# Kernel tuning notes

Hardware: AMD Instinct MI355X
Metric: run time of the kernel (lower is better)

Reference implementation:

```python
import jax, jax.numpy as jnp
import numpy as np

EPS = 1e-12

def _l2norm(x):
    # normalize rows so dot product == cosine similarity
    return x / jnp.maximum(jnp.linalg.norm(x, axis=-1, keepdims=True), EPS)

def setup_inputs() -> dict:
    key = jax.random.key(0)
    k1, k2 = jax.random.split(key)
    source_feats = jax.random.normal(k1, (4096, 1024), dtype=jnp.float32)
    target_feats = jax.random.normal(k2, (65536, 1024), dtype=jnp.float32)
    return {"source_feats": source_feats, "target_feats": target_feats, "k": 4}

def reference(source_feats, target_feats, k):
    # cosine kNN matching: for each source frame, find k nearest target frames
    # by cosine distance, then average the (raw) target features.
    sn = _l2norm(source_feats)           # [N, d]
    tn = _l2norm(target_feats)           # [M, d]
    sim = sn @ tn.T                      # [N, M] cosine similarity (dist = 1 - sim)
    _, idx = jax.lax.top_k(sim, k)       # [N, k] highest similarity == smallest cosine distance
    neighbors = target_feats[idx]        # [N, k, d] gather
    out = neighbors.mean(axis=1)         # [N, d]
    return out
```

## Files before the change

kernel.cpp:

```cpp
#include <hip/hip_runtime.h>
#include <math.h>
#include <stdint.h>

#define M     4096
#define NTGT  65536
#define KD    1024

#define NS    32
#define SLICE (NTGT / NS)
#define BT    256
#define BS    256
#define NTILE (SLICE / BT)
#define TSTEP 16
#define TOTST (NTILE * TSTEP)
#define NCAND 256
#define RESC  32
#define BUFSZ 32768

typedef __attribute__((ext_vector_type(4)))  int i32x4;
typedef __attribute__((ext_vector_type(16))) int i32x16;

__device__ __forceinline__ char f2i8(float x) {
    int t = __float2int_rn(x);
    t = t > 127 ? 127 : (t < -127 ? -127 : t);
    return (char)t;
}

template <int NK>
__device__ __forceinline__ void insert_desc_u(uint32_t (&arr)[NK], uint32_t pk) {
    uint32_t cur = pk;
#pragma unroll
    for (int s = 0; s < NK; ++s) {
        uint32_t old = arr[s];
        bool g = cur > old;
        arr[s] = g ? cur : old;
        cur    = g ? old : cur;
    }
}

__device__ __forceinline__ void gload16(const void* g, void* l) {
    __builtin_amdgcn_global_load_lds(
        (const __attribute__((address_space(1))) unsigned int*)g,
        (__attribute__((address_space(3))) unsigned int*)l, 16, 0, 0);
}

__global__ void prep_targets(const float* __restrict__ T, float* __restrict__ tinv,
                             char* __restrict__ Tq) {
    const int wave = threadIdx.x >> 6;
    const int lane = threadIdx.x & 63;
    const int row  = blockIdx.x * 4 + wave;
    const float* p = T + (size_t)row * KD;
    float4 v[4];
    float s = 0.f;
#pragma unroll
    for (int j = 0; j < 4; ++j) {
        v[j] = *reinterpret_cast<const float4*>(p + lane * 4 + j * 256);
        s += v[j].x * v[j].x + v[j].y * v[j].y + v[j].z * v[j].z + v[j].w * v[j].w;
    }
#pragma unroll
    for (int off = 32; off; off >>= 1) s += __shfl_xor(s, off);
    const float rinv = 1.0f / sqrtf(fmaxf(s, 1e-24f));
    if (lane == 0) tinv[row] = rinv;
    const float sc = rinv * 1024.0f;
#pragma unroll
    for (int j = 0; j < 4; ++j) {
        char4 o;
        o.x = f2i8(v[j].x * sc); o.y = f2i8(v[j].y * sc);
        o.z = f2i8(v[j].z * sc); o.w = f2i8(v[j].w * sc);
        *reinterpret_cast<char4*>(Tq + (size_t)row * KD + lane * 4 + j * 256) = o;
    }
}

__global__ void prep_source(const float* __restrict__ S, char* __restrict__ Sq) {
    const int wave = threadIdx.x >> 6;
    const int lane = threadIdx.x & 63;
    const int row  = blockIdx.x * 4 + wave;
    const float* p = S + (size_t)row * KD;
#pragma unroll
    for (int j = 0; j < 4; ++j) {
        float4 v = *reinterpret_cast<const float4*>(p + lane * 4 + j * 256);
        char4 o;
        o.x = f2i8(v.x * 32.0f); o.y = f2i8(v.y * 32.0f);
        o.z = f2i8(v.z * 32.0f); o.w = f2i8(v.w * 32.0f);
        *reinterpret_cast<char4*>(Sq + (size_t)row * KD + lane * 4 + j * 256) = o;
    }
}

__global__ __launch_bounds__(512, 2)
void screen_kernel(const char* __restrict__ Sq, const char* __restrict__ Tq,
                   uint32_t* __restrict__ cand_out) {
    __shared__ __align__(16) unsigned char lds[2 * BUFSZ];

    const int tid  = threadIdx.x;
    const int lane = tid & 63, wid = tid >> 6;
    const int wr = wid >> 2, wc = wid & 3;
    const int l31 = lane & 31, l5 = lane >> 5;
    const int bx = blockIdx.x;
    const int by = blockIdx.y;
    const int sb   = bx * BS;
    const int tgt0 = by * SLICE;

    const int srow = tid >> 2;
    const int scol = ((tid & 3) ^ ((tid >> 3) & 3)) * 16;
    const char* aStage = Tq + (size_t)(tgt0 + srow) * KD + scol;
    const char* bStage = Sq + (size_t)(sb   + srow) * KD + scol;

    const int s3 = (l31 >> 1) & 3;
    int aOff0[4], aOff1[4], bOff0[2], bOff1[2];
#pragma unroll
    for (int m = 0; m < 4; ++m) {
        const int base = (wr * 128 + m * 32 + l31) * 64;
        aOff0[m] = base + ((l5    ) ^ s3) * 16;
        aOff1[m] = base + ((2 + l5) ^ s3) * 16;
    }
#pragma unroll
    for (int nt = 0; nt < 2; ++nt) {
        const int base = 16384 + (wc * 64 + nt * 32 + l31) * 64;
        bOff0[nt] = base + ((l5    ) ^ s3) * 16;
        bOff1[nt] = base + ((2 + l5) ^ s3) * 16;
    }

#define BARX()  __builtin_amdgcn_s_barrier()
#define FENCE() asm volatile("" ::: "memory")
#define VM4()   asm volatile("s_waitcnt vmcnt(4)" ::: "memory")
#define VM0()   asm volatile("s_waitcnt vmcnt(0)" ::: "memory")

#define STAGE(s_) do {                                                         \
        const int tt_ = (s_) >> 4, ks_ = (s_) & 15;                            \
        unsigned char* d_ = lds + (((s_) & 1) ? BUFSZ : 0) + tid * 16;         \
        const char* a_ = aStage + (size_t)(tt_ * BT) * KD + ks_ * 64;          \
        const char* b_ = bStage + ks_ * 64;                                    \
        gload16(a_,            d_);                                            \
        gload16(a_ + 128 * KD, d_ + 8192);                                     \
        gload16(b_,            d_ + 16384);                                    \
        gload16(b_ + 128 * KD, d_ + 16384 + 8192);                             \
    } while (0)

    uint32_t cand[2][8];
#pragma unroll
    for (int nt = 0; nt < 2; ++nt)
#pragma unroll
        for (int j = 0; j < 8; ++j) cand[nt][j] = 0u;

    STAGE(0);

#pragma unroll 1
    for (int tt = 0; tt < NTILE; ++tt) {
        i32x16 acc[4][2];
#pragma unroll
        for (int m = 0; m < 4; ++m)
#pragma unroll
            for (int nt = 0; nt < 2; ++nt)
                acc[m][nt] = (i32x16){0,0,0,0, 0,0,0,0, 0,0,0,0, 0,0,0,0};

#pragma unroll 1
        for (int ks = 0; ks < TSTEP; ++ks) {
            const int s = tt * TSTEP + ks;
            if (s + 1 < TOTST) { STAGE(s + 1); VM4(); }
            else               { VM0(); }
            BARX(); FENCE();

            const unsigned char* cb = lds + ((s & 1) ? BUFSZ : 0);
            i32x4 a0[4], a1[4], b0[2], b1[2];
#pragma unroll
            for (int m = 0; m < 4; ++m) {
                a0[m] = *reinterpret_cast<const i32x4*>(cb + aOff0[m]);
                a1[m] = *reinterpret_cast<const i32x4*>(cb + aOff1[m]);
            }
#pragma unroll
            for (int nt = 0; nt < 2; ++nt) {
                b0[nt] = *reinterpret_cast<const i32x4*>(cb + bOff0[nt]);
                b1[nt] = *reinterpret_cast<const i32x4*>(cb + bOff1[nt]);
            }
#pragma unroll
            for (int m = 0; m < 4; ++m)
#pragma unroll
                for (int nt = 0; nt < 2; ++nt) {
                    acc[m][nt] = __builtin_amdgcn_mfma_i32_32x32x32_i8(a0[m], b0[nt], acc[m][nt], 0, 0, 0);
                    acc[m][nt] = __builtin_amdgcn_mfma_i32_32x32x32_i8(a1[m], b1[nt], acc[m][nt], 0, 0, 0);
                }

            FENCE(); BARX();
        }

        const int tb = tgt0 + tt * BT;
#pragma unroll
        for (int nt = 0; nt < 2; ++nt) {
            uint32_t c7 = cand[nt][7];
#pragma unroll
            for (int m = 0; m < 4; ++m) {
#pragma unroll
                for (int r = 0; r < 16; ++r) {
                    const int sc = acc[m][nt][r];
                    int k = (sc + (1 << 20)) >> 5;
                    k = k < 0 ? 0 : (k > 65535 ? 65535 : k);
                    const int tg = tb + wr * 128 + m * 32 + (r & 3) + 8 * (r >> 2) + 4 * l5;
                    const uint32_t pk = ((uint32_t)k << 16) | (uint32_t)(tg & 0xFFFF);
                    if (pk > c7) {
                        insert_desc_u<8>(cand[nt], pk);
                        c7 = cand[nt][7];
                    }
                }
            }
        }
    }
#undef STAGE

#pragma unroll
    for (int nt = 0; nt < 2; ++nt) {
        uint32_t inc[8];
#pragma unroll
        for (int j = 0; j < 8; ++j)
            inc[j] = (uint32_t)__shfl_down((int)cand[nt][j], 32);
        if (lane < 32) {
#pragma unroll
            for (int j = 0; j < 8; ++j)
                if (inc[j] > cand[nt][7]) insert_desc_u<8>(cand[nt], inc[j]);
        }
    }

    __syncthreads();
    uint32_t* mbuf = (uint32_t*)lds;
    if (lane < 32) {
#pragma unroll
        for (int nt = 0; nt < 2; ++nt) {
            const int sc = wc * 64 + nt * 32 + l31;
#pragma unroll
            for (int j = 0; j < 8; ++j) mbuf[sc * 16 + wr * 8 + j] = cand[nt][j];
        }
    }
    __syncthreads();

    if (tid < BS) {
        uint32_t best[8];
#pragma unroll
        for (int j = 0; j < 8; ++j) best[j] = 0u;
        const uint32_t* rowp = mbuf + tid * 16;
#pragma unroll
        for (int c = 0; c < 16; ++c) {
            const uint32_t pk = rowp[c];
            if (pk > best[7]) insert_desc_u<8>(best, pk);
        }
        uint32_t* dst = cand_out + (size_t)(sb + tid) * NCAND + by * 8;
#pragma unroll
        for (int j = 0; j < 8; ++j) dst[j] = best[j];
    }
}

__global__ __launch_bounds__(256)
void final_kernel(const uint32_t* __restrict__ cand_out, const float* __restrict__ S,
                  const float* __restrict__ T, const float* __restrict__ tinv,
                  float* __restrict__ out) {
    __shared__ __align__(16) float srow[KD];
    __shared__ float rv[RESC];
    __shared__ int   ri[RESC];
    __shared__ int   sel[4];

    const int r = blockIdx.x;
    const int tid = threadIdx.x;

    *reinterpret_cast<float4*>(srow + tid * 4) =
        *reinterpret_cast<const float4*>(S + (size_t)r * KD + tid * 4);

    if (tid < 64) {
        const uint4 cv = *reinterpret_cast<const uint4*>(cand_out + (size_t)r * NCAND + tid * 4);
        uint32_t c0 = cv.x, c1 = cv.y, c2 = cv.z, c3 = cv.w;
#pragma unroll 1
        for (int it = 0; it < RESC; ++it) {
            uint32_t m01 = c0 > c1 ? c0 : c1;
            uint32_t m23 = c2 > c3 ? c2 : c3;
            uint32_t m = m01 > m23 ? m01 : m23;
#pragma unroll
            for (int off = 32; off; off >>= 1) {
                const uint32_t o = (uint32_t)__shfl_xor((int)m, off);
                m = m > o ? m : o;
            }
            if (tid == 0) ri[it] = (int)(m & 0xFFFFu);
            if      (c0 == m) c0 = 0u;
            else if (c1 == m) c1 = 0u;
            else if (c2 == m) c2 = 0u;
            else if (c3 == m) c3 = 0u;
        }
    }
    __syncthreads();

    const int lane = tid & 63, wv = tid >> 6;
    for (int c = wv; c < RESC; c += 4) {
        const int idx = ri[c];
        const float* tp = T + (size_t)idx * KD;
        float s = 0.f;
#pragma unroll
        for (int j = 0; j < 4; ++j) {
            const float4 tv = *reinterpret_cast<const float4*>(tp + lane * 4 + j * 256);
            const float4 sv = *reinterpret_cast<const float4*>(srow + lane * 4 + j * 256);
            s += tv.x * sv.x + tv.y * sv.y + tv.z * sv.z + tv.w * sv.w;
        }
#pragma unroll
        for (int off = 32; off; off >>= 1) s += __shfl_xor(s, off);
        if (lane == 0) rv[c] = s * tinv[idx];
    }
    __syncthreads();

    if (tid == 0) {
        float b0 = -INFINITY, b1 = -INFINITY, b2 = -INFINITY, b3 = -INFINITY;
        int s0 = 0, s1 = 0, s2 = 0, s3 = 0;
        for (int c = 0; c < RESC; ++c) {
            const float v = rv[c]; const int id = ri[c];
            if (v > b3) {
                if (v > b0)      { b3=b2;s3=s2; b2=b1;s2=s1; b1=b0;s1=s0; b0=v;s0=id; }
                else if (v > b1) { b3=b2;s3=s2; b2=b1;s2=s1; b1=v;s1=id; }
                else if (v > b2) { b3=b2;s3=s2; b2=v;s2=id; }
                else             { b3=v;s3=id; }
            }
        }
        sel[0]=s0; sel[1]=s1; sel[2]=s2; sel[3]=s3;
    }
    __syncthreads();

    float4 a = make_float4(0.f, 0.f, 0.f, 0.f);
#pragma unroll
    for (int q = 0; q < 4; ++q) {
        const float4 v = *reinterpret_cast<const float4*>(T + (size_t)sel[q] * KD + tid * 4);
        a.x += v.x; a.y += v.y; a.z += v.z; a.w += v.w;
    }
    a.x *= 0.25f; a.y *= 0.25f; a.z *= 0.25f; a.w *= 0.25f;
    *reinterpret_cast<float4*>(out + (size_t)r * KD + tid * 4) = a;
}

#define FNS    32
#define FSLICE (NTGT / FNS)
#define FBM 128
#define FBN 128
#define FBK 16
#define FNTILE (FSLICE / FBN)
#define FLDA 132
#define FLDSS 33

__global__ void tinv_kernel(const float* __restrict__ T, float* __restrict__ tinv) {
    const int wave = threadIdx.x >> 6;
    const int lane = threadIdx.x & 63;
    const int row  = blockIdx.x * 4 + wave;
    const float* p = T + (size_t)row * KD;
    float s = 0.f;
#pragma unroll
    for (int j = 0; j < 4; ++j) {
        float4 v = *reinterpret_cast<const float4*>(p + lane * 4 + j * 256);
        s += v.x * v.x + v.y * v.y + v.z * v.z + v.w * v.w;
    }
#pragma unroll
    for (int off = 32; off; off >>= 1) s += __shfl_xor(s, off);
    if (lane == 0) tinv[row] = 1.0f / sqrtf(fmaxf(s, 1e-24f));
}

__global__ __launch_bounds__(256, 2)
void simtopk_kernel(const float* __restrict__ S, const float* __restrict__ T,
                    const float* __restrict__ tinv,
                    float* __restrict__ pval, int* __restrict__ pidx) {
    __shared__ float smem[2 * FBK * FLDA];
    __shared__ float tinvS[FBN];
    float* As = smem;
    float* Bs = smem + FBK * FLDA;
    float* Ss = smem;

    const int tid = threadIdx.x;
    const int tx = tid & 15, ty = tid >> 4;
    const int rb   = blockIdx.x;
    const int tgt0 = blockIdx.y * FSLICE;
    const size_t abase = (size_t)(rb * FBM) * KD;

    float t0 = -INFINITY, t1 = -INFINITY, t2 = -INFINITY, t3 = -INFINITY;
    int   i0 = 0, i1 = 0, i2 = 0, i3 = 0;

    for (int nt = 0; nt < FNTILE; ++nt) {
        const int tb = tgt0 + nt * FBN;
        float acc[8][8];
#pragma unroll
        for (int i = 0; i < 8; ++i)
#pragma unroll
            for (int j = 0; j < 8; ++j) acc[i][j] = 0.f;

        for (int kk = 0; kk < KD; kk += FBK) {
            const int rr = tid >> 2;
            const int c4 = (tid & 3) * 4;
#pragma unroll
            for (int h = 0; h < 2; ++h) {
                const int row = rr + h * 64;
                float4 av = *reinterpret_cast<const float4*>(S + abase + (size_t)row * KD + kk + c4);
                float4 bv = *reinterpret_cast<const float4*>(T + (size_t)(tb + row) * KD + kk + c4);
                As[(c4 + 0) * FLDA + row] = av.x; As[(c4 + 1) * FLDA + row] = av.y;
                As[(c4 + 2) * FLDA + row] = av.z; As[(c4 + 3) * FLDA + row] = av.w;
                Bs[(c4 + 0) * FLDA + row] = bv.x; Bs[(c4 + 1) * FLDA + row] = bv.y;
                Bs[(c4 + 2) * FLDA + row] = bv.z; Bs[(c4 + 3) * FLDA + row] = bv.w;
            }
            __syncthreads();
#pragma unroll
            for (int k = 0; k < FBK; ++k) {
                float a[8], b[8];
                *reinterpret_cast<float4*>(&a[0]) = *reinterpret_cast<float4*>(&As[k * FLDA + ty * 8]);
                *reinterpret_cast<float4*>(&a[4]) = *reinterpret_cast<float4*>(&As[k * FLDA + ty * 8 + 4]);
                *reinterpret_cast<float4*>(&b[0]) = *reinterpret_cast<float4*>(&Bs[k * FLDA + tx * 4]);
                *reinterpret_cast<float4*>(&b[4]) = *reinterpret_cast<float4*>(&Bs[k * FLDA + 64 + tx * 4]);
#pragma unroll
                for (int i = 0; i < 8; ++i)
#pragma unroll
                    for (int j = 0; j < 8; ++j)
                        acc[i][j] = fmaf(a[i], b[j], acc[i][j]);
            }
            __syncthreads();
        }

        if (tid < FBN) tinvS[tid] = tinv[tb + tid];
        __syncthreads();

#pragma unroll
        for (int cc = 0; cc < 4; ++cc) {
            const int g = cc >> 1;
            if ((tx >> 3) == (cc & 1)) {
                const int txl = tx & 7;
#pragma unroll
                for (int i = 0; i < 8; ++i) {
                    const int rrow = ty * 8 + i;
#pragma unroll
                    for (int j = 0; j < 4; ++j) {
                        const int colc = 4 * txl + j;
                        Ss[rrow * FLDSS + colc] = acc[i][g * 4 + j] * tinvS[cc * 32 + colc];
                    }
                }
            }
            __syncthreads();
            if (tid < FBM) {
#pragma unroll 4
                for (int c = 0; c < 32; ++c) {
                    const float v = Ss[tid * FLDSS + c];
                    if (v > t3) {
                        const int gi = tb + cc * 32 + c;
                        if (v > t0)      { t3=t2;i3=i2; t2=t1;i2=i1; t1=t0;i1=i0; t0=v;i0=gi; }
                        else if (v > t1) { t3=t2;i3=i2; t2=t1;i2=i1; t1=v;i1=gi; }
                        else if (v > t2) { t3=t2;i3=i2; t2=v;i2=gi; }
                        else             { t3=v;i3=gi; }
                    }
                }
            }
            __syncthreads();
        }
    }

    if (tid < FBM) {
        const int row = rb * FBM + tid;
        const size_t base = ((size_t)blockIdx.y * M + row) * 4;
        pval[base + 0] = t0; pval[base + 1] = t1; pval[base + 2] = t2; pval[base + 3] = t3;
        pidx[base + 0] = i0; pidx[base + 1] = i1; pidx[base + 2] = i2; pidx[base + 3] = i3;
    }
}

__global__ void merge_kernel(const float* __restrict__ pval, const int* __restrict__ pidx,
                             const float* __restrict__ T, float* __restrict__ out) {
    __shared__ float cv[FNS * 4];
    __shared__ int   ci[FNS * 4];
    __shared__ int   sel[4];
    const int r = blockIdx.x;
    const int tid = threadIdx.x;

    if (tid < FNS * 4) {
        const int s = tid >> 2, q = tid & 3;
        const size_t base = ((size_t)s * M + r) * 4 + q;
        cv[tid] = pval[base];
        ci[tid] = pidx[base];
    }
    __syncthreads();

    if (tid == 0) {
        float t0 = -INFINITY, t1 = -INFINITY, t2 = -INFINITY, t3 = -INFINITY;
        int   j0 = 0, j1 = 0, j2 = 0, j3 = 0;
        for (int c = 0; c < FNS * 4; ++c) {
            const float v = cv[c];
            if (v > t3) {
                const int gi = ci[c];
                if (v > t0)      { t3=t2;j3=j2; t2=t1;j2=j1; t1=t0;j1=j0; t0=v;j0=gi; }
                else if (v > t1) { t3=t2;j3=j2; t2=t1;j2=j1; t1=v;j1=gi; }
                else if (v > t2) { t3=t2;j3=j2; t2=v;j2=gi; }
                else             { t3=v;j3=gi; }
            }
        }
        sel[0] = j0; sel[1] = j1; sel[2] = j2; sel[3] = j3;
    }
    __syncthreads();

    const int d = tid * 4;
    float4 a = make_float4(0.f, 0.f, 0.f, 0.f);
#pragma unroll
    for (int q = 0; q < 4; ++q) {
        const float4 v = *reinterpret_cast<const float4*>(T + (size_t)sel[q] * KD + d);
        a.x += v.x; a.y += v.y; a.z += v.z; a.w += v.w;
    }
    a.x *= 0.25f; a.y *= 0.25f; a.z *= 0.25f; a.w *= 0.25f;
    *reinterpret_cast<float4*>(out + (size_t)r * KD + d) = a;
}

extern "C" void kernel_launch(void* const* d_in, const int* in_sizes, int n_in,
                              void* d_out, int out_size, void* d_ws, size_t ws_size,
                              hipStream_t stream) {
    const float* S = (const float*)d_in[0];
    const float* T = (const float*)d_in[1];
    float* out = (float*)d_out;

    const size_t sz_tinv = (size_t)NTGT * 4;
    const size_t sz_Sq   = (size_t)M * KD;
    const size_t sz_Tq   = (size_t)NTGT * KD;
    const size_t sz_cand = (size_t)M * NCAND * 4;
    const size_t need = sz_tinv + sz_Sq + sz_Tq + sz_cand;

    if (ws_size >= need) {
        float*    tinv = (float*)d_ws;
        char*     Sq   = (char*)d_ws + sz_tinv;
        char*     Tq   = (char*)d_ws + sz_tinv + sz_Sq;
        uint32_t* cand = (uint32_t*)((char*)d_ws + sz_tinv + sz_Sq + sz_Tq);

        prep_targets<<<NTGT / 4, 256, 0, stream>>>(T, tinv, Tq);
        prep_source<<<M / 4, 256, 0, stream>>>(S, Sq);
        screen_kernel<<<dim3(M / BS, NS), 512, 0, stream>>>(Sq, Tq, cand);
        final_kernel<<<M, 256, 0, stream>>>(cand, S, T, tinv, out);
    } else {
        float* tinv = (float*)d_ws;
        float* pval = tinv + NTGT;
        int*   pidx = (int*)(pval + (size_t)FNS * M * 4);

        tinv_kernel<<<NTGT / 4, 256, 0, stream>>>(T, tinv);
        simtopk_kernel<<<dim3(M / FBM, FNS), 256, 0, stream>>>(S, T, tinv, pval, pidx);
        merge_kernel<<<M, 256, 0, stream>>>(pval, pidx, T, out);
    }
}
```

Before: 566.5 us.

## Software-pipeline LDS fragment reads with MFMA using register double buffering

Restructures the int8 MFMA main loop so the LDS fragment reads for the next K-step are issued before the MFMAs of the current step, using even/odd register fragment sets and a loop unrolled by two. Global prefetch now runs two stages ahead into the two LDS buffers. The goal is to hide LDS read latency behind matrix-core work. In exchange it doubles the fragment register footprint, which may lower occupancy, and it changes the buffer-reuse ordering, which the barriers must still keep correct.

```diff
diff --git a/kernel.cpp b/kernel.cpp
--- a/kernel.cpp
+++ b/kernel.cpp
@@ -124,6 +124,7 @@
 #define FENCE() asm volatile("" ::: "memory")
 #define VM4()   asm volatile("s_waitcnt vmcnt(4)" ::: "memory")
 #define VM0()   asm volatile("s_waitcnt vmcnt(0)" ::: "memory")
+#define LGKM0() asm volatile("s_waitcnt lgkmcnt(0)" ::: "memory")
 
 #define STAGE(s_) do {                                                         \
         const int tt_ = (s_) >> 4, ks_ = (s_) & 15;                            \
@@ -136,13 +137,41 @@
         gload16(b_ + 128 * KD, d_ + 16384 + 8192);                             \
     } while (0)
 
+#define READF(A0, A1, B0, B1, CB) do {                                         \
+        _Pragma("unroll")                                                      \
+        for (int m = 0; m < 4; ++m) {                                          \
+            A0[m] = *reinterpret_cast<const i32x4*>((CB) + aOff0[m]);          \
+            A1[m] = *reinterpret_cast<const i32x4*>((CB) + aOff1[m]);          \
+        }                                                                      \
+        _Pragma("unroll")                                                      \
+        for (int nt = 0; nt < 2; ++nt) {                                       \
+            B0[nt] = *reinterpret_cast<const i32x4*>((CB) + bOff0[nt]);        \
+            B1[nt] = *reinterpret_cast<const i32x4*>((CB) + bOff1[nt]);        \
+        } } while (0)
+
+#define MFMAS(A0, A1, B0, B1) do {                                             \
+        _Pragma("unroll")                                                      \
+        for (int m = 0; m < 4; ++m)                                            \
+            _Pragma("unroll")                                                  \
+            for (int nt = 0; nt < 2; ++nt) {                                   \
+                acc[m][nt] = __builtin_amdgcn_mfma_i32_32x32x32_i8(A0[m], B0[nt], acc[m][nt], 0, 0, 0); \
+                acc[m][nt] = __builtin_amdgcn_mfma_i32_32x32x32_i8(A1[m], B1[nt], acc[m][nt], 0, 0, 0); \
+            } } while (0)
+
     uint32_t cand[2][8];
 #pragma unroll
     for (int nt = 0; nt < 2; ++nt)
 #pragma unroll
         for (int j = 0; j < 8; ++j) cand[nt][j] = 0u;
 
-    STAGE(0);
+    i32x4 aE0[4], aE1[4], bE0[2], bE1[2];
+    i32x4 aO0[4], aO1[4], bO0[2], bO1[2];
+
+    STAGE(0); STAGE(1);
+    VM4();
+    BARX(); FENCE();
+    READF(aE0, aE1, bE0, bE1, lds);
+    LGKM0(); FENCE(); BARX();
 
 #pragma unroll 1
     for (int tt = 0; tt < NTILE; ++tt) {
@@ -154,33 +183,28 @@
                 acc[m][nt] = (i32x16){0,0,0,0, 0,0,0,0, 0,0,0,0, 0,0,0,0};
 
 #pragma unroll 1
-        for (int ks = 0; ks < TSTEP; ++ks) {
-            const int s = tt * TSTEP + ks;
-            if (s + 1 < TOTST) { STAGE(s + 1); VM4(); }
-            else               { VM0(); }
-            BARX(); FENCE();
-
-            const unsigned char* cb = lds + ((s & 1) ? BUFSZ : 0);
-            i32x4 a0[4], a1[4], b0[2], b1[2];
-#pragma unroll
-            for (int m = 0; m < 4; ++m) {
-                a0[m] = *reinterpret_cast<const i32x4*>(cb + aOff0[m]);
-                a1[m] = *reinterpret_cast<const i32x4*>(cb + aOff1[m]);
-            }
-#pragma unroll
-            for (int nt = 0; nt < 2; ++nt) {
-                b0[nt] = *reinterpret_cast<const i32x4*>(cb + bOff0[nt]);
-                b1[nt] = *reinterpret_cast<const i32x4*>(cb + bOff1[nt]);
-            }
-#pragma unroll
-            for (int m = 0; m < 4; ++m)
-#pragma unroll
-                for (int nt = 0; nt < 2; ++nt) {
-                    acc[m][nt] = __builtin_amdgcn_mfma_i32_32x32x32_i8(a0[m], b0[nt], acc[m][nt], 0, 0, 0);
-                    acc[m][nt] = __builtin_amdgcn_mfma_i32_32x32x32_i8(a1[m], b1[nt], acc[m][nt], 0, 0, 0);
-                }
-
-            FENCE(); BARX();
+        for (int kp = 0; kp < TSTEP / 2; ++kp) {
+            const int s0 = tt * TSTEP + kp * 2;
+            {
+                const int s = s0;
+                const bool st = (s + 2) < TOTST;
+                if (st) { STAGE(s + 2); VM4(); } else { VM0(); }
+                BARX(); FENCE();
+                READF(aO0, aO1, bO0, bO1, lds + BUFSZ);
+                MFMAS(aE0, aE1, bE0, bE1);
+                LGKM0(); FENCE(); BARX();
+            }
+            {
+                const int s = s0 + 1;
+                const bool st = (s + 2) < TOTST;
+                const bool rd = (s + 1) < TOTST;
+                if (st) { STAGE(s + 2); VM4(); }
+                else if (rd) { VM0(); }
+                BARX(); FENCE();
+                if (rd) READF(aE0, aE1, bE0, bE1, lds);
+                MFMAS(aO0, aO1, bO0, bO1);
+                LGKM0(); FENCE(); BARX();
+            }
         }
 
         const int tb = tgt0 + tt * BT;
@@ -205,6 +229,8 @@
         }
     }
 #undef STAGE
+#undef READF
+#undef MFMAS
 
 #pragma unroll
     for (int nt = 0; nt < 2; ++nt) {
```

Result: slower. 761.4 us (+34.4%).

## Shrink screen tile to 128 targets with 4 waves, drop cross-wave candidate merge

Applied to the files above, without the earlier changes.

Halves the target tile height and the block size to 256 threads (4 waves each covering all 128 target rows), so the per-wave candidate lists no longer need an LDS merge across wave rows and are written straight to global memory. The staging layout and the wait count change to match, with each block now loading 6 chunks per step (2 target, 4 source). This cuts the epilogue barriers and merge work and shrinks LDS use, which may allow more blocks per CU. In exchange each target tile is read twice as many times relative to source reuse, and there is less MFMA work per block to hide memory latency.

```diff
diff --git a/kernel.cpp b/kernel.cpp
--- a/kernel.cpp
+++ b/kernel.cpp
@@ -8,14 +8,14 @@
 
 #define NS    32
 #define SLICE (NTGT / NS)
-#define BT    256
+#define BT    128
 #define BS    256
 #define NTILE (SLICE / BT)
 #define TSTEP 16
 #define TOTST (NTILE * TSTEP)
 #define NCAND 256
 #define RESC  32
-#define BUFSZ 32768
+#define BUFSZ 24576
 
 typedef __attribute__((ext_vector_type(4)))  int i32x4;
 typedef __attribute__((ext_vector_type(16))) int i32x16;
@@ -86,14 +86,13 @@
     }
 }
 
-__global__ __launch_bounds__(512, 2)
+__global__ __launch_bounds__(256, 2)
 void screen_kernel(const char* __restrict__ Sq, const char* __restrict__ Tq,
                    uint32_t* __restrict__ cand_out) {
     __shared__ __align__(16) unsigned char lds[2 * BUFSZ];
 
     const int tid  = threadIdx.x;
-    const int lane = tid & 63, wid = tid >> 6;
-    const int wr = wid >> 2, wc = wid & 3;
+    const int lane = tid & 63, wc = tid >> 6;
     const int l31 = lane & 31, l5 = lane >> 5;
     const int bx = blockIdx.x;
     const int by = blockIdx.y;
@@ -109,20 +108,20 @@
     int aOff0[4], aOff1[4], bOff0[2], bOff1[2];
 #pragma unroll
     for (int m = 0; m < 4; ++m) {
-        const int base = (wr * 128 + m * 32 + l31) * 64;
+        const int base = (m * 32 + l31) * 64;
         aOff0[m] = base + ((l5    ) ^ s3) * 16;
         aOff1[m] = base + ((2 + l5) ^ s3) * 16;
     }
 #pragma unroll
     for (int nt = 0; nt < 2; ++nt) {
-        const int base = 16384 + (wc * 64 + nt * 32 + l31) * 64;
+        const int base = 8192 + (wc * 64 + nt * 32 + l31) * 64;
         bOff0[nt] = base + ((l5    ) ^ s3) * 16;
         bOff1[nt] = base + ((2 + l5) ^ s3) * 16;
     }
 
 #define BARX()  __builtin_amdgcn_s_barrier()
 #define FENCE() asm volatile("" ::: "memory")
-#define VM4()   asm volatile("s_waitcnt vmcnt(4)" ::: "memory")
+#define VM6()   asm volatile("s_waitcnt vmcnt(6)" ::: "memory")
 #define VM0()   asm volatile("s_waitcnt vmcnt(0)" ::: "memory")
 
 #define STAGE(s_) do {                                                         \
@@ -131,9 +130,11 @@
         const char* a_ = aStage + (size_t)(tt_ * BT) * KD + ks_ * 64;          \
         const char* b_ = bStage + ks_ * 64;                                    \
         gload16(a_,            d_);                                            \
-        gload16(a_ + 128 * KD, d_ + 8192);                                     \
-        gload16(b_,            d_ + 16384);                                    \
-        gload16(b_ + 128 * KD, d_ + 16384 + 8192);                             \
+        gload16(a_ + 64 * KD,  d_ + 4096);                                     \
+        gload16(b_,            d_ + 8192);                                     \
+        gload16(b_ + 64 * KD,  d_ + 8192 + 4096);                              \
+        gload16(b_ + 128 * KD, d_ + 8192 + 8192);                              \
+        gload16(b_ + 192 * KD, d_ + 8192 + 12288);                             \
     } while (0)
 
     uint32_t cand[2][8];
@@ -156,7 +157,7 @@
 #pragma unroll 1
         for (int ks = 0; ks < TSTEP; ++ks) {
             const int s = tt * TSTEP + ks;
-            if (s + 1 < TOTST) { STAGE(s + 1); VM4(); }
+            if (s + 1 < TOTST) { STAGE(s + 1); VM6(); }
             else               { VM0(); }
             BARX(); FENCE();
 
@@ -194,7 +195,7 @@
                     const int sc = acc[m][nt][r];
                     int k = (sc + (1 << 20)) >> 5;
                     k = k < 0 ? 0 : (k > 65535 ? 65535 : k);
-                    const int tg = tb + wr * 128 + m * 32 + (r & 3) + 8 * (r >> 2) + 4 * l5;
+                    const int tg = tb + m * 32 + (r & 3) + 8 * (r >> 2) + 4 * l5;
                     const uint32_t pk = ((uint32_t)k << 16) | (uint32_t)(tg & 0xFFFF);
                     if (pk > c7) {
                         insert_desc_u<8>(cand[nt], pk);
@@ -219,31 +220,14 @@
         }
     }
 
-    __syncthreads();
-    uint32_t* mbuf = (uint32_t*)lds;
     if (lane < 32) {
 #pragma unroll
         for (int nt = 0; nt < 2; ++nt) {
-            const int sc = wc * 64 + nt * 32 + l31;
-#pragma unroll
-            for (int j = 0; j < 8; ++j) mbuf[sc * 16 + wr * 8 + j] = cand[nt][j];
-        }
-    }
-    __syncthreads();
-
-    if (tid < BS) {
-        uint32_t best[8];
-#pragma unroll
-        for (int j = 0; j < 8; ++j) best[j] = 0u;
-        const uint32_t* rowp = mbuf + tid * 16;
-#pragma unroll
-        for (int c = 0; c < 16; ++c) {
-            const uint32_t pk = rowp[c];
-            if (pk > best[7]) insert_desc_u<8>(best, pk);
-        }
-        uint32_t* dst = cand_out + (size_t)(sb + tid) * NCAND + by * 8;
-#pragma unroll
-        for (int j = 0; j < 8; ++j) dst[j] = best[j];
+            const int src = sb + wc * 64 + nt * 32 + l31;
+            uint32_t* dst = cand_out + (size_t)src * NCAND + by * 8;
+            *reinterpret_cast<uint4*>(dst)     = make_uint4(cand[nt][0], cand[nt][1], cand[nt][2], cand[nt][3]);
+            *reinterpret_cast<uint4*>(dst + 4) = make_uint4(cand[nt][4], cand[nt][5], cand[nt][6], cand[nt][7]);
+        }
     }
 }
 
@@ -518,7 +502,7 @@
 
         prep_targets<<<NTGT / 4, 256, 0, stream>>>(T, tinv, Tq);
         prep_source<<<M / 4, 256, 0, stream>>>(S, Sq);
-        screen_kernel<<<dim3(M / BS, NS), 512, 0, stream>>>(Sq, Tq, cand);
+        screen_kernel<<<dim3(M / BS, NS), 256, 0, stream>>>(Sq, Tq, cand);
         final_kernel<<<M, 256, 0, stream>>>(cand, S, T, tinv, out);
     } else {
         float* tinv = (float*)d_ws;
```

After: 517.8 us. -8.6%, faster.
